# Kernel optimization log

Measured on AMD Instinct MI355X. Metric: run time of the kernel, lower is better.

Reference implementation:

```python
import math
import jax, jax.numpy as jnp
import numpy as np

D_MODEL = 512
NUM_HEADS = 8
FACTOR = 128
B, T = 16, 768


def setup_inputs() -> dict:
    key = jax.random.key(0)
    ks = jax.random.split(key, 8)
    s_in = 1.0 / math.sqrt(D_MODEL)
    x = jax.random.normal(ks[0], (B, T, D_MODEL), dtype=jnp.float32)
    Wqkv = jax.random.normal(ks[1], (3 * D_MODEL, D_MODEL), dtype=jnp.float32) * s_in
    bqkv = jax.random.normal(ks[2], (3 * D_MODEL,), dtype=jnp.float32) * s_in
    Wconv = jax.random.normal(ks[3], (D_MODEL, D_MODEL, 3), dtype=jnp.float32) * (1.0 / math.sqrt(3 * D_MODEL))
    bconv = jax.random.normal(ks[4], (D_MODEL,), dtype=jnp.float32) * s_in
    gamma = jnp.ones((D_MODEL,), dtype=jnp.float32)
    beta = jnp.zeros((D_MODEL,), dtype=jnp.float32)
    return {"x": x, "Wqkv": Wqkv, "bqkv": bqkv, "Wconv": Wconv, "bconv": bconv, "gamma": gamma, "beta": beta}


def reference(x, Wqkv, bqkv, Wconv, bconv, gamma, beta):
    Bq, Tq, D = x.shape
    H, dk = NUM_HEADS, D // NUM_HEADS
    # --- ProbAttention ---
    qkv = x @ Wqkv.T + bqkv                         # [B,T,3D]
    q, k, v = jnp.split(qkv, 3, axis=-1)
    q = q.reshape(Bq, Tq, H, dk).transpose(0, 2, 1, 3)   # [B,H,T,dk]
    k = k.reshape(Bq, Tq, H, dk).transpose(0, 2, 1, 3)
    v = v.reshape(Bq, Tq, H, dk).transpose(0, 2, 1, 3)
    U = FACTOR * int(math.log(Tq))                  # == T for our config
    scores = jnp.einsum('bhqd,bhkd->bhqk', q, k) / math.sqrt(dk)  # [B,H,T,T]
    top_vals, _ = jax.lax.top_k(scores, U)          # descending-sorted, like torch.topk
    attn = jax.nn.softmax(top_vals, axis=-1)        # [B,H,T,U]
    out = jnp.einsum('bhqu,bhud->bhqd', attn, v)    # requires U == T, as in torch
    attn_out = out.transpose(0, 2, 1, 3).reshape(Bq, Tq, D)
    # --- strided conv branch: Conv1d(D, D, k=3, s=2, p=1) ---
    xc = x.transpose(0, 2, 1)                       # [B,D,T]
    yc = jax.lax.conv_general_dilated(xc, Wconv, window_strides=(2,), padding=[(1, 1)],
                                      dimension_numbers=('NCH', 'OIH', 'NCH'))
    yc = yc + bconv[None, :, None]
    x_conv = yc.transpose(0, 2, 1)                  # [B,T//2,D]
    # --- residual + LayerNorm ---
    res = attn_out[:, ::2, :] + x_conv
    mu = jnp.mean(res, axis=-1, keepdims=True)
    var = jnp.mean(jnp.square(res - mu), axis=-1, keepdims=True)
    y = (res - mu) * jax.lax.rsqrt(var + 1e-5) * gamma + beta
    return y  # dropout is identity in eval mode
```

## Files before the change

### kernel.cpp

```cpp
#include <hip/hip_runtime.h>
#include <hip/hip_bf16.h>
#include <hip/hip_fp16.h>
#include <stdint.h>
#include <math.h>

#define TSEQ 768
#define TOUT 384
#define DM   512
#define NH   8
#define DKH  64

typedef short bf16x8 __attribute__((ext_vector_type(8)));
typedef float f32x4  __attribute__((ext_vector_type(4)));
typedef __fp16 f16x2 __attribute__((ext_vector_type(2)));

__device__ __forceinline__ unsigned short f2bf(float f){
  unsigned int u = __float_as_uint(f);
  unsigned int r = (u + 0x7FFFu + ((u >> 16) & 1u)) >> 16;
  return (unsigned short)r;
}

#define MFMA(a,b,c) __builtin_amdgcn_mfma_f32_16x16x32_bf16((a),(b),(c),0,0,0)

typedef __attribute__((address_space(1))) const void* gas_ptr;
typedef __attribute__((address_space(3))) void*       las_ptr;
__device__ __forceinline__ void gload16(const void* g, void* l){
  __builtin_amdgcn_global_load_lds((gas_ptr)g, (las_ptr)l, 16, 0, 0);
}

__device__ __forceinline__ unsigned xlane_xor_u(unsigned x, int dl){
  int xi = (int)x;
  if (dl == 1)      return (unsigned)__builtin_amdgcn_update_dpp(xi, xi, 0xB1, 0xF, 0xF, true);
  else if (dl == 2) return (unsigned)__builtin_amdgcn_update_dpp(xi, xi, 0x4E, 0xF, 0xF, true);
  else if (dl == 4) return (unsigned)__builtin_amdgcn_ds_swizzle(xi, 0x101F);
  else if (dl == 8) return (unsigned)__builtin_amdgcn_update_dpp(xi, xi, 0x128, 0xF, 0xF, true);
  else return (unsigned)__shfl_xor(xi, dl, 64);
}
__device__ __forceinline__ float xlane_xor_f(float x, int dl){
  return __int_as_float((int)xlane_xor_u((unsigned)__float_as_int(x), dl));
}

__device__ __forceinline__ unsigned pmax2(unsigned a, unsigned b){
  f16x2 r = __builtin_elementwise_max(*reinterpret_cast<f16x2*>(&a),
                                      *reinterpret_cast<f16x2*>(&b));
  return *reinterpret_cast<unsigned*>(&r);
}
__device__ __forceinline__ unsigned pmin2(unsigned a, unsigned b){
  f16x2 r = __builtin_elementwise_min(*reinterpret_cast<f16x2*>(&a),
                                      *reinterpret_cast<f16x2*>(&b));
  return *reinterpret_cast<unsigned*>(&r);
}
__device__ __forceinline__ unsigned pkrtz(float a, float b){
  f16x2 h = __builtin_amdgcn_cvt_pkrtz(a, b);
  return *reinterpret_cast<unsigned*>(&h);
}
__device__ __forceinline__ float lo16f(unsigned u){
  f16x2 h = *reinterpret_cast<f16x2*>(&u); return (float)h[0];
}
__device__ __forceinline__ float hi16f(unsigned u){
  f16x2 h = *reinterpret_cast<f16x2*>(&u); return (float)h[1];
}

__global__ __launch_bounds__(256) void k_cvt(const float* __restrict__ in,
                                             unsigned short* __restrict__ out, int n){
  int i = (blockIdx.x * 256 + threadIdx.x) * 8;
  if (i >= n) return;
  float4 a = *reinterpret_cast<const float4*>(in + i);
  float4 b = *reinterpret_cast<const float4*>(in + i + 4);
  unsigned short u[8] = {f2bf(a.x),f2bf(a.y),f2bf(a.z),f2bf(a.w),
                         f2bf(b.x),f2bf(b.y),f2bf(b.z),f2bf(b.w)};
  *reinterpret_cast<bf16x8*>(out + i) = *reinterpret_cast<bf16x8*>(u);
}

__global__ __launch_bounds__(256) void k_cvt_wconv(const float* __restrict__ w,
                                                   unsigned short* __restrict__ o){
  int idx = blockIdx.x * 256 + threadIdx.x;
  float w0 = w[idx*3+0], w1 = w[idx*3+1], w2 = w[idx*3+2];
  o[idx]          = f2bf(w0);
  o[262144 + idx] = f2bf(w1);
  o[524288 + idx] = f2bf(w2);
}

__global__ __launch_bounds__(256) void k_qkv(const unsigned short* __restrict__ xb,
    const unsigned short* __restrict__ wq, const float* __restrict__ bias,
    unsigned short* __restrict__ qe, unsigned short* __restrict__ kb,
    unsigned short* __restrict__ vb){
  __shared__ unsigned short sA[128*32];
  __shared__ unsigned short sB[128*32];
  int bm = blockIdx.x % 96, bn = blockIdx.x / 96;
  int m0 = bm*128, n0 = bn*128;
  int tid = threadIdx.x, w = tid>>6, l = tid&63;
  int wr = w>>1, wc = w&1, lr = l&15, lk = (l>>4)*8;

  int srow = w*32 + (l>>2);
  int scol = (l&3)*8;
  const unsigned short* gA = xb + (size_t)(m0 + srow)*DM + scol;
  const unsigned short* gB = wq + (size_t)(n0 + srow)*DM + scol;
  unsigned short* dA = sA + w*1024;
  unsigned short* dB = sB + w*1024;

  const unsigned short* ra = sA + (wr*64 + lr)*32 + lk;
  const unsigned short* rb = sB + (wc*64 + lr)*32 + lk;

  f32x4 z = {0.f,0.f,0.f,0.f};
  f32x4 acc[4][4] = {{z,z,z,z},{z,z,z,z},{z,z,z,z},{z,z,z,z}};

  #pragma unroll 1
  for (int ks=0; ks<16; ++ks){
    int k0 = ks*32;
    gload16(gA + k0,          dA);
    gload16(gA + 16*DM + k0,  dA + 512);
    gload16(gB + k0,          dB);
    gload16(gB + 16*DM + k0,  dB + 512);
    __syncthreads();
    bf16x8 af[4], bfr[4];
    #pragma unroll
    for (int f=0; f<4; ++f){
      af[f]  = *reinterpret_cast<const bf16x8*>(ra + f*512);
      bfr[f] = *reinterpret_cast<const bf16x8*>(rb + f*512);
    }
    #pragma unroll
    for (int fq=0; fq<4; ++fq)
      #pragma unroll
      for (int fn=0; fn<4; ++fn)
        acc[fq][fn] = MFMA(af[fq], bfr[fn], acc[fq][fn]);
    __syncthreads();
  }

  int region = n0 >> 9;
  #pragma unroll
  for (int fq=0; fq<4; ++fq)
    #pragma unroll
    for (int fn=0; fn<4; ++fn)
      #pragma unroll
      for (int r=0; r<4; ++r){
        int m = m0 + wr*64 + fq*16 + (l>>4)*4 + r;
        int b = m / TSEQ, t = m - b*TSEQ;
        int n = n0 + wc*64 + fn*16 + lr;
        float val = acc[fq][fn][r] + bias[n];
        unsigned short bv = f2bf(val);
        int bh = b*NH + ((n>>6)&7); int d = n & 63;
        if (region == 0){ if((t&1)==0) qe[((size_t)bh*TOUT + (t>>1))*DKH + d] = bv; }
        else if (region == 1){ kb[((size_t)bh*TSEQ + t)*DKH + d] = bv; }
        else { vb[((size_t)bh*TSEQ + t)*DKH + d] = bv; }
      }
}

__global__ __launch_bounds__(256) void k_vt(const unsigned short* __restrict__ vb,
                                            unsigned short* __restrict__ vT){
  __shared__ unsigned short tile[64][72];
  int bh = blockIdx.x / 12, tt = blockIdx.x % 12;
  int t0 = tt*64;
  int tid = threadIdx.x;
  int r = tid >> 2, c0 = (tid & 3) * 16;
  const unsigned short* src = vb + ((size_t)bh*TSEQ + t0 + r)*DKH + c0;
  *reinterpret_cast<bf16x8*>(&tile[r][c0])   = *reinterpret_cast<const bf16x8*>(src);
  *reinterpret_cast<bf16x8*>(&tile[r][c0+8]) = *reinterpret_cast<const bf16x8*>(src + 8);
  __syncthreads();
  int d = r;
  unsigned short tmp[16];
  #pragma unroll
  for (int j=0;j<16;++j) tmp[j] = tile[c0+j][d];
  unsigned short* dst = vT + ((size_t)bh*DKH + d)*TSEQ + t0 + c0;
  *reinterpret_cast<bf16x8*>(dst)     = *reinterpret_cast<bf16x8*>(tmp);
  *reinterpret_cast<bf16x8*>(dst + 8) = *reinterpret_cast<bf16x8*>(tmp + 8);
}

#define SQ_ROWB 3088
__global__ __launch_bounds__(512, 4) void k_attn(const unsigned short* __restrict__ qe,
    const unsigned short* __restrict__ kb, const unsigned short* __restrict__ vT,
    float* __restrict__ attn){
  __shared__ alignas(16) char sq_raw[16*SQ_ROWB];
  int bh = blockIdx.x / 24, qb = blockIdx.x % 24;
  int tid = threadIdx.x, w = tid>>6, l = tid&63, lr = l&15, lk = (l>>4)*8;

  const unsigned short* qbase = qe + ((size_t)bh*TOUT + qb*16)*DKH;
  bf16x8 qa0 = *reinterpret_cast<const bf16x8*>(qbase + lr*DKH + lk);
  bf16x8 qa1 = *reinterpret_cast<const bf16x8*>(qbase + lr*DKH + 32 + lk);
  const unsigned short* kbase = kb + (size_t)bh*TSEQ*DKH;
  #pragma unroll
  for (int i=0;i<6;++i){
    int nt = w + 8*i;
    const unsigned short* kr = kbase + (size_t)(nt*16 + lr)*DKH + lk;
    bf16x8 B0 = *reinterpret_cast<const bf16x8*>(kr);
    bf16x8 B1 = *reinterpret_cast<const bf16x8*>(kr + 32);
    f32x4 c = {0.f,0.f,0.f,0.f};
    c = MFMA(qa0,B0,c);
    c = MFMA(qa1,B1,c);
    int col = nt*16 + lr;
    int A = col*4;
    int sw = A ^ (((A >> 8) & 7) << 4);
    #pragma unroll
    for (int r=0;r<4;++r){
      int qr = (l>>4)*4 + r;
      *reinterpret_cast<float*>(sq_raw + qr*SQ_ROWB + sw) = c[r] * 0.125f;
    }
  }
  __syncthreads();

  {
    char* rowA = sq_raw + (w*2)*SQ_ROWB;
    char* rowB = rowA + SQ_ROWB;
    unsigned wv[16];
    if (l < 48){
      #pragma unroll
      for (int i4=0;i4<4;++i4){
        int A = l*64 + i4*16;
        int Asw = A ^ (((A >> 8) & 7) << 4);
        f32x4 va = *reinterpret_cast<f32x4*>(rowA + Asw);
        f32x4 vb = *reinterpret_cast<f32x4*>(rowB + Asw);
        wv[i4*4+0] = pkrtz(va[0], vb[0]);
        wv[i4*4+1] = pkrtz(va[1], vb[1]);
        wv[i4*4+2] = pkrtz(va[2], vb[2]);
        wv[i4*4+3] = pkrtz(va[3], vb[3]);
      }
    } else {
      #pragma unroll
      for (int j=0;j<16;++j) wv[j] = 0xFC00FC00u;
    }
    int lane16 = l << 4;
    #pragma unroll
    for (int k = 2; k <= 1024; k <<= 1){
      #pragma unroll
      for (int D = k>>1; D >= 16; D >>= 1){
        int dl = D >> 4;
        bool sel = ((lane16 & k) == 0) == ((l & dl) == 0);
        #pragma unroll
        for (int j=0;j<16;++j){
          unsigned y  = xlane_xor_u(wv[j], dl);
          unsigned mx = pmax2(wv[j], y), mn = pmin2(wv[j], y);
          wv[j] = sel ? mx : mn;
        }
      }
      #pragma unroll
      for (int D = ((k>>1) > 8 ? 8 : (k>>1)); D >= 1; D >>= 1){
        #pragma unroll
        for (int j=0;j<16;++j){
          if ((j & D) == 0){
            int j2 = j | D;
            unsigned mx = pmax2(wv[j], wv[j2]), mn = pmin2(wv[j], wv[j2]);
            if (k <= 8){
              if ((j & k) == 0){ wv[j] = mx; wv[j2] = mn; }
              else             { wv[j] = mn; wv[j2] = mx; }
            } else {
              bool up = (k == 16) ? ((l & 1) == 0) : ((lane16 & k) == 0);
              wv[j]  = up ? mx : mn;
              wv[j2] = up ? mn : mx;
            }
          }
        }
      }
    }
    #pragma unroll 1
    for (int half=0; half<2; ++half){
      float xf[16];
      #pragma unroll
      for (int j=0;j<16;++j) xf[j] = half ? hi16f(wv[j]) : lo16f(wv[j]);
      float mx0 = __shfl(xf[0], 0, 64);
      float s = 0.f;
      #pragma unroll
      for (int j=0;j<16;++j){ xf[j] = __expf(xf[j]-mx0); s += xf[j]; }
      #pragma unroll
      for (int o=1;o<64;o<<=1) s += xlane_xor_f(s, o);
      float inv = 1.f / s;
      if (l < 48){
        unsigned short u[16];
        #pragma unroll
        for (int j=0;j<16;++j) u[j] = f2bf(xf[j]*inv);
        char* pp = (half ? rowB : rowA) + l*32;
        *reinterpret_cast<bf16x8*>(pp)      = *reinterpret_cast<bf16x8*>(u);
        *reinterpret_cast<bf16x8*>(pp + 16) = *reinterpret_cast<bf16x8*>(u + 8);
      }
    }
  }
  __syncthreads();

  if (w < 4){
    f32x4 o = {0.f,0.f,0.f,0.f};
    const unsigned short* vtb = vT + ((size_t)bh*DKH + w*16 + lr)*TSEQ + lk;
    const char* prow = sq_raw + lr*SQ_ROWB + (l>>4)*16;
    #pragma unroll
    for (int ks=0; ks<24; ++ks){
      bf16x8 a  = *reinterpret_cast<const bf16x8*>(prow + ks*64);
      bf16x8 bb = *reinterpret_cast<const bf16x8*>(vtb + ks*32);
      o = MFMA(a,bb,o);
    }
    int b = bh >> 3, h = bh & 7;
    float* ab = attn + ((size_t)b*TOUT + qb*16)*DM + h*DKH + w*16 + lr;
    #pragma unroll
    for (int r=0;r<4;++r){
      int qr = (l>>4)*4 + r;
      ab[(size_t)qr*DM] = o[r];
    }
  }
}

__global__ __launch_bounds__(256) void k_conv(const unsigned short* __restrict__ xb,
    const unsigned short* __restrict__ wc, const float* __restrict__ bconv,
    float* __restrict__ res){
  int bm = blockIdx.x % 96, bn = blockIdx.x / 96;
  int m0 = bm*64, n0 = bn*64;
  int tid = threadIdx.x, w = tid>>6, l = tid&63;
  int wr = w>>1, wc2 = w&1, lr = l&15, lk = (l>>4)*8;
  int b = m0 / TOUT, t0 = m0 - b*TOUT;
  f32x4 z = {0.f,0.f,0.f,0.f};
  f32x4 acc00=z, acc01=z, acc10=z, acc11=z;
  int tA0 = t0 + wr*32 + lr;
  const unsigned short* xrow = xb + (size_t)b*TSEQ*DM;
  #pragma unroll 1
  for (int j=0;j<3;++j){
    int tin0 = 2*tA0 + j - 1;
    int tin1 = tin0 + 32;
    bool v0 = (tin0 >= 0);
    const unsigned short* a0p = xrow + (ptrdiff_t)tin0*DM + lk;
    const unsigned short* a1p = xrow + (ptrdiff_t)tin1*DM + lk;
    const unsigned short* w0p = wc + (size_t)j*262144 + (size_t)(n0 + wc2*32 + lr)*DM + lk;
    const unsigned short* w1p = w0p + 16*DM;
    #pragma unroll
    for (int ks=0; ks<16; ++ks){
      bf16x8 A0 = {0,0,0,0,0,0,0,0};
      if (v0) A0 = *reinterpret_cast<const bf16x8*>(a0p + ks*32);
      bf16x8 A1 = *reinterpret_cast<const bf16x8*>(a1p + ks*32);
      bf16x8 B0 = *reinterpret_cast<const bf16x8*>(w0p + ks*32);
      bf16x8 B1 = *reinterpret_cast<const bf16x8*>(w1p + ks*32);
      acc00 = MFMA(A0,B0,acc00);
      acc01 = MFMA(A0,B1,acc01);
      acc10 = MFMA(A1,B0,acc10);
      acc11 = MFMA(A1,B1,acc11);
    }
  }
  #define CONV_STORE(ACC, RB, CB) \
  { _Pragma("unroll") \
    for (int r=0;r<4;++r){ \
      int t = t0 + wr*32 + (RB)*16 + (l>>4)*4 + r; \
      int n = n0 + wc2*32 + (CB)*16 + lr; \
      size_t idx = ((size_t)b*TOUT + t)*DM + n; \
      res[idx] = ACC[r] + bconv[n] + res[idx]; } }
  CONV_STORE(acc00,0,0) CONV_STORE(acc01,0,1) CONV_STORE(acc10,1,0) CONV_STORE(acc11,1,1)
  #undef CONV_STORE
}

__global__ __launch_bounds__(256) void k_ln(const float* __restrict__ res,
    const float* __restrict__ gamma, const float* __restrict__ beta,
    float* __restrict__ out){
  int row = blockIdx.x*4 + (threadIdx.x>>6);
  int l = threadIdx.x & 63;
  const float* rp = res + (size_t)row*DM + l*8;
  float4 v0 = *reinterpret_cast<const float4*>(rp);
  float4 v1 = *reinterpret_cast<const float4*>(rp + 4);
  float s = v0.x+v0.y+v0.z+v0.w + v1.x+v1.y+v1.z+v1.w;
  #pragma unroll
  for (int o=1;o<64;o<<=1) s += __shfl_xor(s, o, 64);
  float mean = s * (1.f/512.f);
  float d0=v0.x-mean, d1=v0.y-mean, d2=v0.z-mean, d3=v0.w-mean;
  float d4=v1.x-mean, d5=v1.y-mean, d6=v1.z-mean, d7=v1.w-mean;
  float q = d0*d0+d1*d1+d2*d2+d3*d3+d4*d4+d5*d5+d6*d6+d7*d7;
  #pragma unroll
  for (int o=1;o<64;o<<=1) q += __shfl_xor(q, o, 64);
  float var = q * (1.f/512.f);
  float inv = rsqrtf(var + 1e-5f);
  float4 g0 = *reinterpret_cast<const float4*>(gamma + l*8);
  float4 g1 = *reinterpret_cast<const float4*>(gamma + l*8 + 4);
  float4 b0 = *reinterpret_cast<const float4*>(beta + l*8);
  float4 b1 = *reinterpret_cast<const float4*>(beta + l*8 + 4);
  float4 o0, o1;
  o0.x = d0*inv*g0.x + b0.x; o0.y = d1*inv*g0.y + b0.y;
  o0.z = d2*inv*g0.z + b0.z; o0.w = d3*inv*g0.w + b0.w;
  o1.x = d4*inv*g1.x + b1.x; o1.y = d5*inv*g1.y + b1.y;
  o1.z = d6*inv*g1.z + b1.z; o1.w = d7*inv*g1.w + b1.w;
  float* op = out + (size_t)row*DM + l*8;
  *reinterpret_cast<float4*>(op)     = o0;
  *reinterpret_cast<float4*>(op + 4) = o1;
}

extern "C" void kernel_launch(void* const* d_in, const int* in_sizes, int n_in,
                              void* d_out, int out_size, void* d_ws, size_t ws_size,
                              hipStream_t stream){
  const float* x     = (const float*)d_in[0];
  const float* Wqkv  = (const float*)d_in[1];
  const float* bqkv  = (const float*)d_in[2];
  const float* Wconv = (const float*)d_in[3];
  const float* bconv = (const float*)d_in[4];
  const float* gamma = (const float*)d_in[5];
  const float* beta  = (const float*)d_in[6];
  float* out = (float*)d_out;

  char* ws = (char*)d_ws;
  size_t off = 0;
  auto alloc = [&](size_t bytes)->char*{
    char* p = ws + off; off += (bytes + 255) & ~(size_t)255; return p;
  };
  unsigned short* xb  = (unsigned short*)alloc(6291456ull*2);
  unsigned short* wqb = (unsigned short*)alloc(786432ull*2);
  unsigned short* wc3 = (unsigned short*)alloc(786432ull*2);
  unsigned short* qeb = (unsigned short*)alloc(3145728ull*2);
  unsigned short* kbb = (unsigned short*)alloc(6291456ull*2);
  unsigned short* vbb = (unsigned short*)alloc(6291456ull*2);
  unsigned short* vtb = (unsigned short*)alloc(6291456ull*2);
  float*          resb = (float*)alloc(3145728ull*4);

  k_cvt<<<dim3(3072), dim3(256), 0, stream>>>(x, xb, 6291456);
  k_cvt<<<dim3(384),  dim3(256), 0, stream>>>(Wqkv, wqb, 786432);
  k_cvt_wconv<<<dim3(1024), dim3(256), 0, stream>>>(Wconv, wc3);
  k_qkv<<<dim3(1152), dim3(256), 0, stream>>>(xb, wqb, bqkv, qeb, kbb, vbb);
  k_vt<<<dim3(1536), dim3(256), 0, stream>>>(vbb, vtb);
  k_attn<<<dim3(3072), dim3(512), 0, stream>>>(qeb, kbb, vtb, resb);
  k_conv<<<dim3(768), dim3(256), 0, stream>>>(xb, wc3, bconv, resb);
  k_ln<<<dim3(1536), dim3(256), 0, stream>>>(resb, gamma, beta, out);
}
```

Baseline: 275.0 us.

## Tile conv GEMM at 128x128 with LDS staging via direct global-to-LDS loads

```diff
diff --git a/kernel.cpp b/kernel.cpp
--- a/kernel.cpp
+++ b/kernel.cpp
@@ -298,46 +298,73 @@
 __global__ __launch_bounds__(256) void k_conv(const unsigned short* __restrict__ xb,
     const unsigned short* __restrict__ wc, const float* __restrict__ bconv,
     float* __restrict__ res){
-  int bm = blockIdx.x % 96, bn = blockIdx.x / 96;
-  int m0 = bm*64, n0 = bn*64;
+  __shared__ unsigned short sA[128*32];
+  __shared__ unsigned short sB[128*32];
+  int bm = blockIdx.x % 48, bn = blockIdx.x / 48;
+  int m0 = bm*128, n0 = bn*128;
   int tid = threadIdx.x, w = tid>>6, l = tid&63;
   int wr = w>>1, wc2 = w&1, lr = l&15, lk = (l>>4)*8;
   int b = m0 / TOUT, t0 = m0 - b*TOUT;
+
+  int srow = w*32 + (l>>2);
+  int scol = (l&3)*8;
+  const unsigned short* xrow = xb + (size_t)b*TSEQ*DM;
+  unsigned short* dA = sA + w*1024;
+  unsigned short* dB = sB + w*1024;
+  const unsigned short* ra  = sA + (wr*64 + lr)*32 + lk;
+  const unsigned short* rb_ = sB + (wc2*64 + lr)*32 + lk;
+
   f32x4 z = {0.f,0.f,0.f,0.f};
-  f32x4 acc00=z, acc01=z, acc10=z, acc11=z;
-  int tA0 = t0 + wr*32 + lr;
-  const unsigned short* xrow = xb + (size_t)b*TSEQ*DM;
+  f32x4 acc[4][4] = {{z,z,z,z},{z,z,z,z},{z,z,z,z},{z,z,z,z}};
+  bool zfix = (t0 == 0);
+
   #pragma unroll 1
-  for (int j=0;j<3;++j){
-    int tin0 = 2*tA0 + j - 1;
-    int tin1 = tin0 + 32;
-    bool v0 = (tin0 >= 0);
-    const unsigned short* a0p = xrow + (ptrdiff_t)tin0*DM + lk;
-    const unsigned short* a1p = xrow + (ptrdiff_t)tin1*DM + lk;
-    const unsigned short* w0p = wc + (size_t)j*262144 + (size_t)(n0 + wc2*32 + lr)*DM + lk;
-    const unsigned short* w1p = w0p + 16*DM;
-    #pragma unroll
+  for (int j=0; j<3; ++j){
+    int tin0 = 2*(t0 + srow) + j - 1;
+    int tin0c = tin0 < 0 ? 0 : tin0;
+    const unsigned short* gA0 = xrow + (size_t)tin0c*DM + scol;
+    const unsigned short* gA1 = xrow + (size_t)(tin0 + 32)*DM + scol;
+    const unsigned short* gB  = wc + (size_t)j*262144 + (size_t)(n0 + srow)*DM + scol;
+    bool dz = zfix && (j == 0);
+    #pragma unroll 1
     for (int ks=0; ks<16; ++ks){
-      bf16x8 A0 = {0,0,0,0,0,0,0,0};
-      if (v0) A0 = *reinterpret_cast<const bf16x8*>(a0p + ks*32);
-      bf16x8 A1 = *reinterpret_cast<const bf16x8*>(a1p + ks*32);
-      bf16x8 B0 = *reinterpret_cast<const bf16x8*>(w0p + ks*32);
-      bf16x8 B1 = *reinterpret_cast<const bf16x8*>(w1p + ks*32);
-      acc00 = MFMA(A0,B0,acc00);
-      acc01 = MFMA(A0,B1,acc01);
-      acc10 = MFMA(A1,B0,acc10);
-      acc11 = MFMA(A1,B1,acc11);
+      int k0 = ks*32;
+      gload16(gA0 + k0,         dA);
+      gload16(gA1 + k0,         dA + 512);
+      gload16(gB + k0,          dB);
+      gload16(gB + 16*DM + k0,  dB + 512);
+      __syncthreads();
+      if (dz && tid < 4){
+        bf16x8 zz = {0,0,0,0,0,0,0,0};
+        *reinterpret_cast<bf16x8*>(sA + tid*8) = zz;
+      }
+      __syncthreads();
+      bf16x8 af[4], bfr[4];
+      #pragma unroll
+      for (int f=0; f<4; ++f){
+        af[f]  = *reinterpret_cast<const bf16x8*>(ra  + f*512);
+        bfr[f] = *reinterpret_cast<const bf16x8*>(rb_ + f*512);
+      }
+      #pragma unroll
+      for (int fq=0; fq<4; ++fq)
+        #pragma unroll
+        for (int fn=0; fn<4; ++fn)
+          acc[fq][fn] = MFMA(af[fq], bfr[fn], acc[fq][fn]);
+      __syncthreads();
     }
   }
-  #define CONV_STORE(ACC, RB, CB) \
-  { _Pragma("unroll") \
-    for (int r=0;r<4;++r){ \
-      int t = t0 + wr*32 + (RB)*16 + (l>>4)*4 + r; \
-      int n = n0 + wc2*32 + (CB)*16 + lr; \
-      size_t idx = ((size_t)b*TOUT + t)*DM + n; \
-      res[idx] = ACC[r] + bconv[n] + res[idx]; } }
-  CONV_STORE(acc00,0,0) CONV_STORE(acc01,0,1) CONV_STORE(acc10,1,0) CONV_STORE(acc11,1,1)
-  #undef CONV_STORE
+
+  #pragma unroll
+  for (int fq=0; fq<4; ++fq)
+    #pragma unroll
+    for (int fn=0; fn<4; ++fn)
+      #pragma unroll
+      for (int r=0; r<4; ++r){
+        int t = t0 + wr*64 + fq*16 + (l>>4)*4 + r;
+        int n = n0 + wc2*64 + fn*16 + lr;
+        size_t idx = ((size_t)b*TOUT + t)*DM + n;
+        res[idx] = acc[fq][fn][r] + bconv[n] + res[idx];
+      }
 }
 
 __global__ __launch_bounds__(256) void k_ln(const float* __restrict__ res,
@@ -405,6 +432,6 @@
   k_qkv<<<dim3(1152), dim3(256), 0, stream>>>(xb, wqb, bqkv, qeb, kbb, vbb);
   k_vt<<<dim3(1536), dim3(256), 0, stream>>>(vbb, vtb);
   k_attn<<<dim3(3072), dim3(512), 0, stream>>>(qeb, kbb, vtb, resb);
-  k_conv<<<dim3(768), dim3(256), 0, stream>>>(xb, wc3, bconv, resb);
+  k_conv<<<dim3(192), dim3(256), 0, stream>>>(xb, wc3, bconv, resb);
   k_ln<<<dim3(1536), dim3(256), 0, stream>>>(resb, gamma, beta, out);
 }
```

Result: faster. 240.7 us (-12.5%).
